# Kernel optimization log

Hardware: AMD Instinct MI355X
Metric: run time of the kernel (lower is better)

Reference implementation:

```python
import jax, jax.numpy as jnp
import numpy as np

WL, FL = 64, 40
SCALE = 2.0 ** FL
CLIP_MAX = 2.0 ** (WL - FL - 1) - 2.0 ** (-FL)  # (2^(wl-1)-1)/2^fl
CLIP_MIN = -(2.0 ** (WL - FL - 1))
EPS = 1e-5
H = 8  # num_heads


def quant(x):
    # Fixed-point nearest-rounding quantizer: wl=64, fl=40.
    return jnp.clip(jnp.round(x * SCALE) / SCALE, CLIP_MIN, CLIP_MAX)


def setup_inputs() -> dict:
    key = jax.random.key(0)
    ks = jax.random.split(key, 9)
    N, S, C = 4096, 31, 512  # S = num_particles + 1 = 31 (hard-coded in module)
    SS = S * S
    return {
        "x": jax.random.normal(ks[0], (N, S, C), dtype=jnp.float32),
        "norm_gamma": jnp.ones((C,), jnp.float32),
        "norm_beta": jnp.zeros((C,), jnp.float32),
        "wq": jax.random.normal(ks[1], (C, C), jnp.float32) * 0.02,
        "wk": jax.random.normal(ks[2], (C, C), jnp.float32) * 0.02,
        "wv": jax.random.normal(ks[3], (C, C), jnp.float32) * 0.02,
        "wo": jax.random.normal(ks[4], (C, C), jnp.float32) * 0.02,
        "bo": jnp.zeros((C,), jnp.float32),
        "pre_gamma": jnp.ones((SS,), jnp.float32),
        "pre_beta": jnp.zeros((SS,), jnp.float32),
    }


def reference(x, norm_gamma, norm_beta, wq, wk, wv, wo, bo, pre_gamma, pre_beta):
    N, S, C = x.shape
    # BatchNorm1d(C) on x.transpose(1,2): per-channel stats over (batch, seq), training-mode (batch stats)
    mu = jnp.mean(x, axis=(0, 1))
    var = jnp.var(x, axis=(0, 1))
    out = quant((x - mu) * jax.lax.rsqrt(var + EPS) * norm_gamma + norm_beta)

    out_q = quant(out @ wq.T)
    out_k = quant(out @ wk.T)
    out_v = quant(out @ wv.T)

    q_ = out_q.reshape(N, S, H, C // H)
    k_ = out_k.reshape(N, S, H, C // H)
    v_ = out_v.reshape(N, S, H, C // H)

    energy = quant(jnp.einsum('nqhc,nkhc->nhqk', q_, k_))  # [N,H,S,S]

    # pre_exp_norm: BatchNorm1d(S*S) over reshaped energies; channel dim = S*S, stats over (batch, heads)
    e = energy.reshape(N, H, S * S)
    em = jnp.mean(e, axis=(0, 1))
    ev = jnp.var(e, axis=(0, 1))
    en = quant((e - em) * jax.lax.rsqrt(ev + EPS) * pre_gamma + pre_beta)
    energy_post = en.reshape(N, H, S, S)

    attention = quant(jax.nn.softmax(energy_post / jnp.sqrt(jnp.float32(C)), axis=-1))

    out = quant(jnp.einsum('nhql,nlhc->nqhc', attention, v_)).reshape(N, S, C)
    out = quant(out @ wo.T + bo)
    return quant(out + x)
```

## Files before the change

### kernel.cpp

```cpp
#include <hip/hip_runtime.h>
#include <cstdint>
#include <cstddef>

#define N_ 4096
#define S_ 31
#define C_ 512
#define H_ 8
#define M_ (N_*S_)
#define NH_ (N_*H_)

typedef unsigned short u16;
typedef unsigned char  u8;
typedef __bf16 v8bf __attribute__((ext_vector_type(8)));
typedef float  v4f  __attribute__((ext_vector_type(4)));
typedef float  v2f  __attribute__((ext_vector_type(2)));
typedef unsigned short v8u __attribute__((ext_vector_type(8)));

#define WS_STATS 2097152
#define WS_Q (WS_STATS + 32768)
#define WS_K (WS_Q + 67108864)
#define WS_V (WS_K + 67108864)

#define SCALE_QK 16.0f
#define SCALE_V  16.0f

__device__ __forceinline__ u16 f2bf(float f) {
  union { float f; unsigned u; } v; v.f = f;
  unsigned r = v.u + 0x7FFFu + ((v.u >> 16) & 1u);
  return (u16)(r >> 16);
}
__device__ __forceinline__ float bf2f(u16 v) {
  union { unsigned u; float f; } w; w.u = ((unsigned)v) << 16; return w.f;
}
__device__ __forceinline__ unsigned enc4(float a, float b, float c, float d) {
  int w = __builtin_amdgcn_cvt_pk_fp8_f32(a, b, 0, false);
  w = __builtin_amdgcn_cvt_pk_fp8_f32(c, d, w, true);
  return (unsigned)w;
}
__device__ __forceinline__ v8bf dec8(uint2 u) {
  v2f p0 = __builtin_amdgcn_cvt_pk_f32_fp8((int)u.x, false);
  v2f p1 = __builtin_amdgcn_cvt_pk_f32_fp8((int)u.x, true);
  v2f p2 = __builtin_amdgcn_cvt_pk_f32_fp8((int)u.y, false);
  v2f p3 = __builtin_amdgcn_cvt_pk_f32_fp8((int)u.y, true);
  v8bf r;
  r[0]=(__bf16)p0[0]; r[1]=(__bf16)p0[1]; r[2]=(__bf16)p1[0]; r[3]=(__bf16)p1[1];
  r[4]=(__bf16)p2[0]; r[5]=(__bf16)p2[1]; r[6]=(__bf16)p3[0]; r[7]=(__bf16)p3[1];
  return r;
}

__global__ void k_init(const float* wq, const float* wk, const float* wv, const float* wo,
                       u16* wbf, float* statsf) {
  int gid = blockIdx.x * 256 + threadIdx.x;
  if (gid < 6144) statsf[gid] = 0.0f;
  int m = gid >> 18, o = gid & 262143;
  int e    = o & 7;
  int lane = (o >> 3) & 63;
  int kk   = (o >> 9) & 15;
  int j16  = o >> 13;
  int j = j16 * 16 + (lane & 15);
  int k = kk * 32 + (lane >> 4) * 8 + e;
  const float* src = (m == 0) ? wq : (m == 1) ? wk : (m == 2) ? wv : wo;
  wbf[(size_t)m * 262144 + o] = f2bf(src[j * 512 + k]);
}

__global__ void __launch_bounds__(512) k_xstats(const float* __restrict__ x, float* statsf) {
  int t = threadIdx.x;
  int c4 = (t & 127) * 4;
  int r0 = blockIdx.x * 512 + (t >> 7) * 128;
  float4 s = {0,0,0,0}, sq = {0,0,0,0};
  const float* p = x + (size_t)r0 * C_ + c4;
  for (int i = 0; i < 128; ++i) {
    float4 v = *(const float4*)(p + (size_t)i * C_);
    s.x += v.x; s.y += v.y; s.z += v.z; s.w += v.w;
    sq.x += v.x*v.x; sq.y += v.y*v.y; sq.z += v.z*v.z; sq.w += v.w*v.w;
  }
  atomicAdd(&statsf[c4+0], s.x); atomicAdd(&statsf[c4+1], s.y);
  atomicAdd(&statsf[c4+2], s.z); atomicAdd(&statsf[c4+3], s.w);
  atomicAdd(&statsf[512+c4+0], sq.x); atomicAdd(&statsf[512+c4+1], sq.y);
  atomicAdd(&statsf[512+c4+2], sq.z); atomicAdd(&statsf[512+c4+3], sq.w);
}

__global__ void k_finalize_ch(const float* gamma, const float* beta, float* statsf) {
  int c = threadIdx.x;
  float mu  = statsf[c] * (1.0f / (float)M_);
  float var = statsf[512 + c] * (1.0f / (float)M_) - mu * mu;
  float sc  = rsqrtf(var + 1e-5f) * gamma[c];
  statsf[1024 + c] = sc;
  statsf[1536 + c] = beta[c] - mu * sc;
}

__device__ __forceinline__ void gemm64(const u16* sa, const u16* B0, v4f (&acc)[4][4], int lane) {
  #pragma unroll
  for (int m = 0; m < 4; ++m)
    #pragma unroll
    for (int c = 0; c < 4; ++c) acc[m][c] = (v4f){0,0,0,0};
  #pragma unroll 2
  for (int kk = 0; kk < 16; ++kk) {
    v8bf a[4], b[4];
    #pragma unroll
    for (int m = 0; m < 4; ++m)
      a[m] = *(const v8bf*)(sa + ((((kk*4 + m) << 6) | (lane ^ (kk & 7))) << 3));
    #pragma unroll
    for (int c = 0; c < 4; ++c)
      b[c] = *(const v8bf*)(B0 + (size_t)c * 8192 + kk * 512);
    #pragma unroll
    for (int m = 0; m < 4; ++m)
      #pragma unroll
      for (int c = 0; c < 4; ++c)
        acc[m][c] = __builtin_amdgcn_mfma_f32_16x16x32_bf16(a[m], b[c], acc[m][c], 0, 0, 0);
  }
}

__global__ void __launch_bounds__(512, 4)
k_qkv(const float* __restrict__ x, const u16* __restrict__ wbf,
      const float* __restrict__ statsf, u8* __restrict__ eg8, u8* __restrict__ vt) {
  __shared__ float s_scale[C_], s_shift[C_];
  __shared__ u16 s_a[16*4*64*8];
  int t = threadIdx.x, nblk = blockIdx.x;
  int wave = t >> 6, lane = t & 63, l15 = lane & 15, quad = lane >> 4;
  s_scale[t] = statsf[1024+t]; s_shift[t] = statsf[1536+t];
  __syncthreads();

  const float* xb = x + (size_t)nblk * 2 * S_ * C_;
  for (int it = 0; it < 8; ++it) {
    int idx = t + it * 512;
    int row = idx >> 6, c8 = (idx & 63) << 3;
    int nl = row >> 5, s = row & 31;
    int kk = c8 >> 5, q4 = (c8 >> 3) & 3, mt = row >> 4, r15 = row & 15;
    u16* dst = s_a + ((((kk*4 + mt) << 6) | ((q4*16 + r15) ^ (kk & 7))) << 3);
    v8u o;
    if (s == 31) { o = (v8u){0,0,0,0,0,0,0,0}; }
    else {
      const float* g = xb + (size_t)(nl * 31 + s) * C_ + c8;
      float4 a = *(const float4*)g, b = *(const float4*)(g + 4);
      o[0]=f2bf(a.x*s_scale[c8+0]+s_shift[c8+0]); o[1]=f2bf(a.y*s_scale[c8+1]+s_shift[c8+1]);
      o[2]=f2bf(a.z*s_scale[c8+2]+s_shift[c8+2]); o[3]=f2bf(a.w*s_scale[c8+3]+s_shift[c8+3]);
      o[4]=f2bf(b.x*s_scale[c8+4]+s_shift[c8+4]); o[5]=f2bf(b.y*s_scale[c8+5]+s_shift[c8+5]);
      o[6]=f2bf(b.z*s_scale[c8+6]+s_shift[c8+6]); o[7]=f2bf(b.w*s_scale[c8+7]+s_shift[c8+7]);
    }
    *(v8u*)dst = o;
  }
  __syncthreads();

  v4f acc[4][4];

  gemm64(s_a, wbf + (size_t)2 * 262144 + (size_t)wave * 32768 + (size_t)lane * 8, acc, lane);
  #pragma unroll
  for (int m = 0; m < 4; ++m) {
    int rbase = m*16 + quad*4;
    int nl = rbase >> 5, s0 = rbase & 31;
    size_t nbase = (size_t)(nblk*2 + nl) * 8;
    #pragma unroll
    for (int c = 0; c < 4; ++c) {
      int d = c*16 + l15;
      unsigned w = enc4(acc[m][c][0]*SCALE_V, acc[m][c][1]*SCALE_V,
                        acc[m][c][2]*SCALE_V, acc[m][c][3]*SCALE_V);
      *(unsigned*)(vt + ((nbase + wave) * 2048) + d*32 + s0) = w;
    }
  }

  unsigned qpack[16];
  gemm64(s_a, wbf + (size_t)0 * 262144 + (size_t)wave * 32768 + (size_t)lane * 8, acc, lane);
  #pragma unroll
  for (int m = 0; m < 4; ++m)
    #pragma unroll
    for (int c = 0; c < 4; ++c)
      qpack[m*4+c] = enc4(acc[m][c][0]*SCALE_QK, acc[m][c][1]*SCALE_QK,
                          acc[m][c][2]*SCALE_QK, acc[m][c][3]*SCALE_QK);

  unsigned kpack[16];
  gemm64(s_a, wbf + (size_t)1 * 262144 + (size_t)wave * 32768 + (size_t)lane * 8, acc, lane);
  #pragma unroll
  for (int m = 0; m < 4; ++m)
    #pragma unroll
    for (int c = 0; c < 4; ++c)
      kpack[m*4+c] = enc4(acc[m][c][0]*SCALE_QK, acc[m][c][1]*SCALE_QK,
                          acc[m][c][2]*SCALE_QK, acc[m][c][3]*SCALE_QK);

  __syncthreads();

  u8* scr = (u8*)s_a + wave * 8192;
  #pragma unroll
  for (int m = 0; m < 4; ++m)
    #pragma unroll
    for (int c = 0; c < 4; ++c) {
      int d = c*16 + l15;
      #pragma unroll
      for (int reg = 0; reg < 4; ++reg) {
        int r = m*16 + quad*4 + reg;
        int dd = d ^ ((r & 7) << 3);
        scr[r*64 + dd]        = (u8)(qpack[m*4+c] >> (reg*8));
        scr[4096 + r*64 + dd] = (u8)(kpack[m*4+c] >> (reg*8));
      }
    }

  const float inv = 1.0f / (SCALE_QK * SCALE_QK);
  #pragma unroll 1
  for (int n = 0; n < 2; ++n) {
    v8bf A[2][2], B[2][2];
    #pragma unroll
    for (int mt = 0; mt < 2; ++mt)
      #pragma unroll
      for (int kk = 0; kk < 2; ++kk) {
        int r = n*32 + mt*16 + l15;
        int dA = (kk*32 + quad*8) ^ ((r & 7) << 3);
        A[mt][kk] = dec8(*(const uint2*)(scr + r*64 + dA));
        B[mt][kk] = dec8(*(const uint2*)(scr + 4096 + r*64 + dA));
      }
    u16* ep = (u16*)(eg8 + (((size_t)(nblk*2 + n) * 8 + wave) * 2048));
    #pragma unroll
    for (int qt = 0; qt < 2; ++qt)
      #pragma unroll
      for (int kt = 0; kt < 2; ++kt) {
        v4f a2 = {0,0,0,0};
        a2 = __builtin_amdgcn_mfma_f32_16x16x32_bf16(A[qt][0], B[kt][0], a2, 0, 0, 0);
        a2 = __builtin_amdgcn_mfma_f32_16x16x32_bf16(A[qt][1], B[kt][1], a2, 0, 0, 0);
        int k = kt*16 + l15;
        #pragma unroll
        for (int reg = 0; reg < 4; ++reg) {
          int q = qt*16 + quad*4 + reg;
          ep[q*32 + k] = f2bf(a2[reg] * inv);
        }
      }
  }
}

__global__ void __launch_bounds__(256) k_estats(const u16* __restrict__ eg, float* statsf) {
  int t = threadIdx.x;
  int r0 = blockIdx.x * 128;
  float s[4] = {0,0,0,0}, sq[4] = {0,0,0,0};
  for (int i = 0; i < 128; ++i) {
    uint2 u = *(const uint2*)(eg + (size_t)(r0 + i) * 1024 + t * 4);
    float v0 = bf2f((u16)(u.x & 0xffff)), v1 = bf2f((u16)(u.x >> 16));
    float v2 = bf2f((u16)(u.y & 0xffff)), v3 = bf2f((u16)(u.y >> 16));
    s[0]+=v0; s[1]+=v1; s[2]+=v2; s[3]+=v3;
    sq[0]+=v0*v0; sq[1]+=v1*v1; sq[2]+=v2*v2; sq[3]+=v3*v3;
  }
  #pragma unroll
  for (int j = 0; j < 4; ++j) {
    atomicAdd(&statsf[2048 + t*4 + j], s[j]);
    atomicAdd(&statsf[3072 + t*4 + j], sq[j]);
  }
}

__global__ void k_finalize_e(const float* pg, const float* pb, float* statsf) {
  int c = threadIdx.x;
  int q = c >> 5, k = c & 31;
  const float invC = 0.04419417382415922f;
  float s2 = 0.f, sh2 = 0.f;
  if (q < 31 && k < 31) {
    int ss = q*31 + k;
    float mu  = statsf[2048 + c] * (1.0f / (float)NH_);
    float var = statsf[3072 + c] * (1.0f / (float)NH_) - mu * mu;
    float sc  = rsqrtf(var + 1e-5f) * pg[ss];
    s2  = sc * invC;
    sh2 = (pb[ss] - mu * sc) * invC;
  }
  statsf[4096 + c] = s2;
  statsf[5120 + c] = sh2;
}

__global__ void __launch_bounds__(512, 4)
k_oproj(const float* __restrict__ x, const u16* __restrict__ wbf,
        const float* __restrict__ statsf, const u16* __restrict__ eg,
        const u8* __restrict__ vt, const float* __restrict__ bo, float* __restrict__ out) {
  __shared__ u16 s_a[16*4*64*8];
  __shared__ u16 s_attn[8][1024];
  int t = threadIdx.x, nblk = blockIdx.x;
  int wave = t >> 6, lane = t & 63, l15 = lane & 15, quad = lane >> 4;

  int q = lane & 31, half = lane >> 5;
  #pragma unroll 1
  for (int tk = 0; tk < 2; ++tk) {
    int task = wave * 2 + tk;
    int nl = task >> 3, h = task & 7;
    size_t nh = (size_t)(nblk*2 + nl) * 8 + h;
    const u16* ep = eg + nh * 1024;
    int cb = q*32 + half*16;
    v8u e0 = *(const v8u*)(ep + cb);
    v8u e1 = *(const v8u*)(ep + cb + 8);
    const float* s2g  = statsf + 4096 + cb;
    const float* sh2g = statsf + 5120 + cb;
    float lg[16];
    #pragma unroll
    for (int j = 0; j < 8; ++j) lg[j]   = bf2f(e0[j]) * s2g[j]   + sh2g[j];
    #pragma unroll
    for (int j = 0; j < 8; ++j) lg[8+j] = bf2f(e1[j]) * s2g[8+j] + sh2g[8+j];
    if (half) lg[15] = -1e30f;
    float mx = lg[0];
    #pragma unroll
    for (int j = 1; j < 16; ++j) mx = fmaxf(mx, lg[j]);
    mx = fmaxf(mx, __shfl_xor(mx, 32));
    float sum = 0.f;
    #pragma unroll
    for (int j = 0; j < 16; ++j) { lg[j] = __expf(lg[j] - mx); sum += lg[j]; }
    sum += __shfl_xor(sum, 32);
    float r = (q == 31) ? 0.f : (1.0f / sum);
    v8u o0, o1;
    #pragma unroll
    for (int j = 0; j < 8; ++j) { o0[j] = f2bf(lg[j] * r); o1[j] = f2bf(lg[8+j] * r); }
    *(v8u*)(&s_attn[wave][cb]) = o0;
    *(v8u*)(&s_attn[wave][cb + 8]) = o1;
    v8bf a0 = *(const v8bf*)(&s_attn[wave][(l15)*32 + quad*8]);
    v8bf a1 = *(const v8bf*)(&s_attn[wave][(16 + l15)*32 + quad*8]);
    const float invV = 1.0f / SCALE_V;
    #pragma unroll
    for (int ct = 0; ct < 4; ++ct) {
      uint2 u = *(const uint2*)(vt + nh*2048 + (ct*16 + l15)*32 + quad*8);
      v8bf b = dec8(u);
      v4f c0 = {0,0,0,0}, c1 = {0,0,0,0};
      c0 = __builtin_amdgcn_mfma_f32_16x16x32_bf16(a0, b, c0, 0, 0, 0);
      c1 = __builtin_amdgcn_mfma_f32_16x16x32_bf16(a1, b, c1, 0, 0, 0);
      int ch = h*64 + ct*16 + l15;
      int kkA = ch >> 5, qA = (ch >> 3) & 3, pA = ch & 7;
      #pragma unroll
      for (int reg = 0; reg < 4; ++reg) {
        int rm = quad*4 + reg;
        s_a[((((kkA*4 + nl*2 + 0) << 6) | (qA*16 + rm)) << 3) + pA] = f2bf(c0[reg] * invV);
        s_a[((((kkA*4 + nl*2 + 1) << 6) | (qA*16 + rm)) << 3) + pA] = f2bf(c1[reg] * invV);
      }
    }
  }
  __syncthreads();

  {
    const u16* B0 = wbf + (size_t)3 * 262144 + (size_t)wave * 32768 + (size_t)lane * 8;
    v4f acc[4][4];
    #pragma unroll
    for (int m = 0; m < 4; ++m)
      #pragma unroll
      for (int c = 0; c < 4; ++c) acc[m][c] = (v4f){0,0,0,0};
    #pragma unroll 2
    for (int kk = 0; kk < 16; ++kk) {
      v8bf a[4], b[4];
      #pragma unroll
      for (int m = 0; m < 4; ++m)
        a[m] = *(const v8bf*)(s_a + ((((kk*4 + m) << 6) | lane) << 3));
      #pragma unroll
      for (int c = 0; c < 4; ++c)
        b[c] = *(const v8bf*)(B0 + (size_t)c * 8192 + kk * 512);
      #pragma unroll
      for (int m = 0; m < 4; ++m)
        #pragma unroll
        for (int c = 0; c < 4; ++c)
          acc[m][c] = __builtin_amdgcn_mfma_f32_16x16x32_bf16(a[m], b[c], acc[m][c], 0, 0, 0);
    }
    #pragma unroll
    for (int m = 0; m < 4; ++m) {
      int rbase = m*16 + quad*4;
      int nl = rbase >> 5, s0 = rbase & 31;
      #pragma unroll
      for (int c = 0; c < 4; ++c) {
        int j = wave*64 + c*16 + l15;
        float bj = bo[j];
        #pragma unroll
        for (int reg = 0; reg < 4; ++reg) {
          int s = s0 + reg;
          if (s < 31) {
            size_t off = (size_t)((nblk*2 + nl) * 31 + s) * C_ + j;
            out[off] = acc[m][c][reg] + bj + x[off];
          }
        }
      }
    }
  }
}

extern "C" void kernel_launch(void* const* d_in, const int* in_sizes, int n_in,
                              void* d_out, int out_size, void* d_ws, size_t ws_size,
                              hipStream_t stream) {
  const float* x     = (const float*)d_in[0];
  const float* gamma = (const float*)d_in[1];
  const float* beta  = (const float*)d_in[2];
  const float* wq    = (const float*)d_in[3];
  const float* wk    = (const float*)d_in[4];
  const float* wv    = (const float*)d_in[5];
  const float* wo    = (const float*)d_in[6];
  const float* bo    = (const float*)d_in[7];
  const float* pg    = (const float*)d_in[8];
  const float* pb    = (const float*)d_in[9];

  char* ws = (char*)d_ws;
  u16*   wbf    = (u16*)ws;
  float* statsf = (float*)(ws + WS_STATS);
  u8*    eg8    = (u8*)(ws + WS_Q);
  u8*    vtp    = (u8*)(ws + WS_V);
  float* outp   = (float*)d_out;

  k_init<<<4096, 256, 0, stream>>>(wq, wk, wv, wo, wbf, statsf);
  k_xstats<<<248, 512, 0, stream>>>(x, statsf);
  k_finalize_ch<<<1, 512, 0, stream>>>(gamma, beta, statsf);
  k_qkv<<<2048, 512, 0, stream>>>(x, wbf, statsf, eg8, vtp);
  k_estats<<<256, 256, 0, stream>>>((const u16*)eg8, statsf);
  k_finalize_e<<<1, 1024, 0, stream>>>(pg, pb, statsf);
  k_oproj<<<2048, 512, 0, stream>>>(x, wbf, statsf, (const u16*)eg8, vtp, bo, outp);
}
```

Baseline: 986.2 us.

## Fuse energy batch-stat accumulation into QKV kernel and vectorize PV LDS stores

Removes the separate k_estats pass, which re-read all energies from global memory. The QKV kernel now accumulates per-position sum and sum of squares in shared memory with LDS atomics, then flushes them to global with atomics once per block. Separately, the PV MFMA operands are swapped so each lane holds four contiguous output channels, which allows packed 4-element LDS stores instead of scalar stores. The fused path adds many LDS atomics and 8 KB of shared memory per block, which may reduce occupancy, and it issues more global atomics in total.

```diff
diff --git a/kernel.cpp b/kernel.cpp
--- a/kernel.cpp
+++ b/kernel.cpp
@@ -15,6 +15,7 @@
 typedef float  v4f  __attribute__((ext_vector_type(4)));
 typedef float  v2f  __attribute__((ext_vector_type(2)));
 typedef unsigned short v8u __attribute__((ext_vector_type(8)));
+typedef unsigned short v4u __attribute__((ext_vector_type(4)));
 
 #define WS_STATS 2097152
 #define WS_Q (WS_STATS + 32768)
@@ -113,12 +114,16 @@
 
 __global__ void __launch_bounds__(512, 4)
 k_qkv(const float* __restrict__ x, const u16* __restrict__ wbf,
-      const float* __restrict__ statsf, u8* __restrict__ eg8, u8* __restrict__ vt) {
+      const float* __restrict__ statsf, float* __restrict__ statsw,
+      u8* __restrict__ eg8, u8* __restrict__ vt) {
   __shared__ float s_scale[C_], s_shift[C_];
   __shared__ u16 s_a[16*4*64*8];
+  __shared__ float s_esum[1024], s_esq[1024];
   int t = threadIdx.x, nblk = blockIdx.x;
   int wave = t >> 6, lane = t & 63, l15 = lane & 15, quad = lane >> 4;
   s_scale[t] = statsf[1024+t]; s_shift[t] = statsf[1536+t];
+  s_esum[t] = 0.f; s_esum[t+512] = 0.f;
+  s_esq[t]  = 0.f; s_esq[t+512]  = 0.f;
   __syncthreads();
 
   const float* xb = x + (size_t)nblk * 2 * S_ * C_;
@@ -219,27 +224,19 @@
         #pragma unroll
         for (int reg = 0; reg < 4; ++reg) {
           int q = qt*16 + quad*4 + reg;
-          ep[q*32 + k] = f2bf(a2[reg] * inv);
+          u16 ev = f2bf(a2[reg] * inv);
+          ep[q*32 + k] = ev;
+          float v = bf2f(ev);
+          atomicAdd(&s_esum[q*32 + k], v);
+          atomicAdd(&s_esq[q*32 + k], v*v);
         }
       }
   }
-}
-
-__global__ void __launch_bounds__(256) k_estats(const u16* __restrict__ eg, float* statsf) {
-  int t = threadIdx.x;
-  int r0 = blockIdx.x * 128;
-  float s[4] = {0,0,0,0}, sq[4] = {0,0,0,0};
-  for (int i = 0; i < 128; ++i) {
-    uint2 u = *(const uint2*)(eg + (size_t)(r0 + i) * 1024 + t * 4);
-    float v0 = bf2f((u16)(u.x & 0xffff)), v1 = bf2f((u16)(u.x >> 16));
-    float v2 = bf2f((u16)(u.y & 0xffff)), v3 = bf2f((u16)(u.y >> 16));
-    s[0]+=v0; s[1]+=v1; s[2]+=v2; s[3]+=v3;
-    sq[0]+=v0*v0; sq[1]+=v1*v1; sq[2]+=v2*v2; sq[3]+=v3*v3;
-  }
-  #pragma unroll
-  for (int j = 0; j < 4; ++j) {
-    atomicAdd(&statsf[2048 + t*4 + j], s[j]);
-    atomicAdd(&statsf[3072 + t*4 + j], sq[j]);
+  __syncthreads();
+  #pragma unroll
+  for (int i = t; i < 1024; i += 512) {
+    atomicAdd(&statsw[2048 + i], s_esum[i]);
+    atomicAdd(&statsw[3072 + i], s_esq[i]);
   }
 }
 
@@ -309,16 +306,19 @@
       uint2 u = *(const uint2*)(vt + nh*2048 + (ct*16 + l15)*32 + quad*8);
       v8bf b = dec8(u);
       v4f c0 = {0,0,0,0}, c1 = {0,0,0,0};
-      c0 = __builtin_amdgcn_mfma_f32_16x16x32_bf16(a0, b, c0, 0, 0, 0);
-      c1 = __builtin_amdgcn_mfma_f32_16x16x32_bf16(a1, b, c1, 0, 0, 0);
-      int ch = h*64 + ct*16 + l15;
-      int kkA = ch >> 5, qA = (ch >> 3) & 3, pA = ch & 7;
+      c0 = __builtin_amdgcn_mfma_f32_16x16x32_bf16(b, a0, c0, 0, 0, 0);
+      c1 = __builtin_amdgcn_mfma_f32_16x16x32_bf16(b, a1, c1, 0, 0, 0);
+      int kkA = h*2 + (ct>>1);
+      int qA  = (ct*2 + (quad>>1)) & 3;
+      int pA  = (quad&1)*4;
+      v4u w0, w1;
       #pragma unroll
       for (int reg = 0; reg < 4; ++reg) {
-        int rm = quad*4 + reg;
-        s_a[((((kkA*4 + nl*2 + 0) << 6) | (qA*16 + rm)) << 3) + pA] = f2bf(c0[reg] * invV);
-        s_a[((((kkA*4 + nl*2 + 1) << 6) | (qA*16 + rm)) << 3) + pA] = f2bf(c1[reg] * invV);
-      }
+        w0[reg] = f2bf(c0[reg] * invV);
+        w1[reg] = f2bf(c1[reg] * invV);
+      }
+      *(v4u*)(&s_a[((((kkA*4 + nl*2 + 0) << 6) | (qA*16 + l15)) << 3) + pA]) = w0;
+      *(v4u*)(&s_a[((((kkA*4 + nl*2 + 1) << 6) | (qA*16 + l15)) << 3) + pA]) = w1;
     }
   }
   __syncthreads();
@@ -390,8 +390,7 @@
   k_init<<<4096, 256, 0, stream>>>(wq, wk, wv, wo, wbf, statsf);
   k_xstats<<<248, 512, 0, stream>>>(x, statsf);
   k_finalize_ch<<<1, 512, 0, stream>>>(gamma, beta, statsf);
-  k_qkv<<<2048, 512, 0, stream>>>(x, wbf, statsf, eg8, vtp);
-  k_estats<<<256, 256, 0, stream>>>((const u16*)eg8, statsf);
+  k_qkv<<<2048, 512, 0, stream>>>(x, wbf, statsf, statsf, eg8, vtp);
   k_finalize_e<<<1, 1024, 0, stream>>>(pg, pb, statsf);
   k_oproj<<<2048, 512, 0, stream>>>(x, wbf, statsf, (const u16*)eg8, vtp, bo, outp);
 }
```

Result: slower. 1.282 ms (+30.0%).

## Double k_qkv row tile to four batch items per block for weight reuse

Applied to the files above, without the earlier changes.

The QKV projection kernel now processes four batch items (128 padded rows) per block instead of two, so each weight fragment loaded from global memory feeds twice as many MFMA tiles. Shared memory for the A tile and the Q/K scratch doubles, accumulators double, launch bounds drop to 2 blocks per CU, and the grid halves. It cuts weight traffic per output row, at the cost of higher register and LDS pressure and lower occupancy.

```diff
diff --git a/kernel.cpp b/kernel.cpp
--- a/kernel.cpp
+++ b/kernel.cpp
@@ -89,45 +89,51 @@
   statsf[1536 + c] = beta[c] - mu * sc;
 }
 
-__device__ __forceinline__ void gemm64(const u16* sa, const u16* B0, v4f (&acc)[4][4], int lane) {
-  #pragma unroll
-  for (int m = 0; m < 4; ++m)
-    #pragma unroll
-    for (int c = 0; c < 4; ++c) acc[m][c] = (v4f){0,0,0,0};
+__device__ __forceinline__ void gemm128(const u16* sa, const u16* B0, v4f (&acc)[2][4][4], int lane) {
+  #pragma unroll
+  for (int h = 0; h < 2; ++h)
+    #pragma unroll
+    for (int m = 0; m < 4; ++m)
+      #pragma unroll
+      for (int c = 0; c < 4; ++c) acc[h][m][c] = (v4f){0,0,0,0};
   #pragma unroll 2
   for (int kk = 0; kk < 16; ++kk) {
-    v8bf a[4], b[4];
-    #pragma unroll
-    for (int m = 0; m < 4; ++m)
-      a[m] = *(const v8bf*)(sa + ((((kk*4 + m) << 6) | (lane ^ (kk & 7))) << 3));
+    v8bf a[2][4], b[4];
     #pragma unroll
     for (int c = 0; c < 4; ++c)
       b[c] = *(const v8bf*)(B0 + (size_t)c * 8192 + kk * 512);
     #pragma unroll
-    for (int m = 0; m < 4; ++m)
-      #pragma unroll
-      for (int c = 0; c < 4; ++c)
-        acc[m][c] = __builtin_amdgcn_mfma_f32_16x16x32_bf16(a[m], b[c], acc[m][c], 0, 0, 0);
-  }
-}
-
-__global__ void __launch_bounds__(512, 4)
+    for (int h = 0; h < 2; ++h)
+      #pragma unroll
+      for (int m = 0; m < 4; ++m)
+        a[h][m] = *(const v8bf*)(sa + ((((kk*8 + h*4 + m) << 6) | (lane ^ (kk & 7))) << 3));
+    #pragma unroll
+    for (int h = 0; h < 2; ++h)
+      #pragma unroll
+      for (int m = 0; m < 4; ++m)
+        #pragma unroll
+        for (int c = 0; c < 4; ++c)
+          acc[h][m][c] = __builtin_amdgcn_mfma_f32_16x16x32_bf16(a[h][m], b[c], acc[h][m][c], 0, 0, 0);
+  }
+}
+
+__global__ void __launch_bounds__(512, 2)
 k_qkv(const float* __restrict__ x, const u16* __restrict__ wbf,
       const float* __restrict__ statsf, u8* __restrict__ eg8, u8* __restrict__ vt) {
   __shared__ float s_scale[C_], s_shift[C_];
-  __shared__ u16 s_a[16*4*64*8];
+  __shared__ u16 s_a[16*8*64*8];
   int t = threadIdx.x, nblk = blockIdx.x;
   int wave = t >> 6, lane = t & 63, l15 = lane & 15, quad = lane >> 4;
   s_scale[t] = statsf[1024+t]; s_shift[t] = statsf[1536+t];
   __syncthreads();
 
-  const float* xb = x + (size_t)nblk * 2 * S_ * C_;
-  for (int it = 0; it < 8; ++it) {
+  const float* xb = x + (size_t)nblk * 4 * S_ * C_;
+  for (int it = 0; it < 16; ++it) {
     int idx = t + it * 512;
     int row = idx >> 6, c8 = (idx & 63) << 3;
     int nl = row >> 5, s = row & 31;
     int kk = c8 >> 5, q4 = (c8 >> 3) & 3, mt = row >> 4, r15 = row & 15;
-    u16* dst = s_a + ((((kk*4 + mt) << 6) | ((q4*16 + r15) ^ (kk & 7))) << 3);
+    u16* dst = s_a + ((((kk*8 + mt) << 6) | ((q4*16 + r15) ^ (kk & 7))) << 3);
     v8u o;
     if (s == 31) { o = (v8u){0,0,0,0,0,0,0,0}; }
     else {
@@ -142,61 +148,69 @@
   }
   __syncthreads();
 
-  v4f acc[4][4];
-
-  gemm64(s_a, wbf + (size_t)2 * 262144 + (size_t)wave * 32768 + (size_t)lane * 8, acc, lane);
-  #pragma unroll
-  for (int m = 0; m < 4; ++m) {
-    int rbase = m*16 + quad*4;
-    int nl = rbase >> 5, s0 = rbase & 31;
-    size_t nbase = (size_t)(nblk*2 + nl) * 8;
-    #pragma unroll
-    for (int c = 0; c < 4; ++c) {
-      int d = c*16 + l15;
-      unsigned w = enc4(acc[m][c][0]*SCALE_V, acc[m][c][1]*SCALE_V,
-                        acc[m][c][2]*SCALE_V, acc[m][c][3]*SCALE_V);
-      *(unsigned*)(vt + ((nbase + wave) * 2048) + d*32 + s0) = w;
+  v4f acc[2][4][4];
+
+  gemm128(s_a, wbf + (size_t)2 * 262144 + (size_t)wave * 32768 + (size_t)lane * 8, acc, lane);
+  #pragma unroll
+  for (int h = 0; h < 2; ++h)
+    #pragma unroll
+    for (int m = 0; m < 4; ++m) {
+      int rbase = h*64 + m*16 + quad*4;
+      int nl = rbase >> 5, s0 = rbase & 31;
+      size_t nbase = (size_t)(nblk*4 + nl) * 8;
+      #pragma unroll
+      for (int c = 0; c < 4; ++c) {
+        int d = c*16 + l15;
+        unsigned w = enc4(acc[h][m][c][0]*SCALE_V, acc[h][m][c][1]*SCALE_V,
+                          acc[h][m][c][2]*SCALE_V, acc[h][m][c][3]*SCALE_V);
+        *(unsigned*)(vt + ((nbase + wave) * 2048) + d*32 + s0) = w;
+      }
     }
-  }
-
-  unsigned qpack[16];
-  gemm64(s_a, wbf + (size_t)0 * 262144 + (size_t)wave * 32768 + (size_t)lane * 8, acc, lane);
-  #pragma unroll
-  for (int m = 0; m < 4; ++m)
-    #pragma unroll
-    for (int c = 0; c < 4; ++c)
-      qpack[m*4+c] = enc4(acc[m][c][0]*SCALE_QK, acc[m][c][1]*SCALE_QK,
-                          acc[m][c][2]*SCALE_QK, acc[m][c][3]*SCALE_QK);
-
-  unsigned kpack[16];
-  gemm64(s_a, wbf + (size_t)1 * 262144 + (size_t)wave * 32768 + (size_t)lane * 8, acc, lane);
-  #pragma unroll
-  for (int m = 0; m < 4; ++m)
-    #pragma unroll
-    for (int c = 0; c < 4; ++c)
-      kpack[m*4+c] = enc4(acc[m][c][0]*SCALE_QK, acc[m][c][1]*SCALE_QK,
-                          acc[m][c][2]*SCALE_QK, acc[m][c][3]*SCALE_QK);
+
+  unsigned qpack[32];
+  gemm128(s_a, wbf + (size_t)0 * 262144 + (size_t)wave * 32768 + (size_t)lane * 8, acc, lane);
+  #pragma unroll
+  for (int h = 0; h < 2; ++h)
+    #pragma unroll
+    for (int m = 0; m < 4; ++m)
+      #pragma unroll
+      for (int c = 0; c < 4; ++c)
+        qpack[h*16 + m*4 + c] = enc4(acc[h][m][c][0]*SCALE_QK, acc[h][m][c][1]*SCALE_QK,
+                                     acc[h][m][c][2]*SCALE_QK, acc[h][m][c][3]*SCALE_QK);
+
+  unsigned kpack[32];
+  gemm128(s_a, wbf + (size_t)1 * 262144 + (size_t)wave * 32768 + (size_t)lane * 8, acc, lane);
+  #pragma unroll
+  for (int h = 0; h < 2; ++h)
+    #pragma unroll
+    for (int m = 0; m < 4; ++m)
+      #pragma unroll
+      for (int c = 0; c < 4; ++c)
+        kpack[h*16 + m*4 + c] = enc4(acc[h][m][c][0]*SCALE_QK, acc[h][m][c][1]*SCALE_QK,
+                                     acc[h][m][c][2]*SCALE_QK, acc[h][m][c][3]*SCALE_QK);
 
   __syncthreads();
 
-  u8* scr = (u8*)s_a + wave * 8192;
-  #pragma unroll
-  for (int m = 0; m < 4; ++m)
-    #pragma unroll
-    for (int c = 0; c < 4; ++c) {
-      int d = c*16 + l15;
-      #pragma unroll
-      for (int reg = 0; reg < 4; ++reg) {
-        int r = m*16 + quad*4 + reg;
-        int dd = d ^ ((r & 7) << 3);
-        scr[r*64 + dd]        = (u8)(qpack[m*4+c] >> (reg*8));
-        scr[4096 + r*64 + dd] = (u8)(kpack[m*4+c] >> (reg*8));
-      }
-    }
+  u8* scr = (u8*)s_a + wave * 16384;
+  #pragma unroll
+  for (int h = 0; h < 2; ++h)
+    #pragma unroll
+    for (int m = 0; m < 4; ++m)
+      #pragma unroll
+      for (int c = 0; c < 4; ++c) {
+        int d = c*16 + l15;
+        #pragma unroll
+        for (int reg = 0; reg < 4; ++reg) {
+          int r = h*64 + m*16 + quad*4 + reg;
+          int dd = d ^ ((r & 7) << 3);
+          scr[r*64 + dd]        = (u8)(qpack[h*16 + m*4 + c] >> (reg*8));
+          scr[8192 + r*64 + dd] = (u8)(kpack[h*16 + m*4 + c] >> (reg*8));
+        }
+      }
 
   const float inv = 1.0f / (SCALE_QK * SCALE_QK);
   #pragma unroll 1
-  for (int n = 0; n < 2; ++n) {
+  for (int n = 0; n < 4; ++n) {
     v8bf A[2][2], B[2][2];
     #pragma unroll
     for (int mt = 0; mt < 2; ++mt)
@@ -205,9 +219,9 @@
         int r = n*32 + mt*16 + l15;
         int dA = (kk*32 + quad*8) ^ ((r & 7) << 3);
         A[mt][kk] = dec8(*(const uint2*)(scr + r*64 + dA));
-        B[mt][kk] = dec8(*(const uint2*)(scr + 4096 + r*64 + dA));
-      }
-    u16* ep = (u16*)(eg8 + (((size_t)(nblk*2 + n) * 8 + wave) * 2048));
+        B[mt][kk] = dec8(*(const uint2*)(scr + 8192 + r*64 + dA));
+      }
+    u16* ep = (u16*)(eg8 + (((size_t)(nblk*4 + n) * 8 + wave) * 2048));
     #pragma unroll
     for (int qt = 0; qt < 2; ++qt)
       #pragma unroll
@@ -390,7 +404,7 @@
   k_init<<<4096, 256, 0, stream>>>(wq, wk, wv, wo, wbf, statsf);
   k_xstats<<<248, 512, 0, stream>>>(x, statsf);
   k_finalize_ch<<<1, 512, 0, stream>>>(gamma, beta, statsf);
-  k_qkv<<<2048, 512, 0, stream>>>(x, wbf, statsf, eg8, vtp);
+  k_qkv<<<1024, 512, 0, stream>>>(x, wbf, statsf, eg8, vtp);
   k_estats<<<256, 256, 0, stream>>>((const u16*)eg8, statsf);
   k_finalize_e<<<1, 1024, 0, stream>>>(pg, pb, statsf);
   k_oproj<<<2048, 512, 0, stream>>>(x, wbf, statsf, (const u16*)eg8, vtp, bo, outp);
```

New measurement: 995.1 us. Within noise of the previous version (+0.9%).
